# Kernel tuning notes

Hardware: AMD Instinct MI355X
Metric: run time of the kernel (lower is better)

Reference implementation:

```python
import jax, jax.numpy as jnp
import numpy as np


def setup_inputs() -> dict:
    key = jax.random.key(0)
    k1, k2 = jax.random.split(key)
    b, c, h, w = 16, 2048, 32, 32
    n_points = 64
    fea = jax.random.normal(k1, (b, c, h, w), dtype=jnp.float32)
    point_list = jax.random.uniform(k2, (n_points, 2), dtype=jnp.float32)  # (x, y) in [0,1)
    valid = jnp.ones((n_points,), dtype=bool)
    return {"fea": fea, "point_list": point_list, "valid": valid}


def reference(fea, point_list, valid):
    # forward_point of SimModel, with fea == backbone(x)['feat4']
    b, c, h, w = fea.shape
    # point_cur = [int(px*w), int(py*h)]  (points in [0,1) so trunc == floor)
    ix = jnp.clip((point_list[:, 0] * w).astype(jnp.int32), 0, w - 1)  # [P]
    iy = jnp.clip((point_list[:, 1] * h).astype(jnp.int32), 0, h - 1)  # [P]
    # gather query feature vectors at each point: [b, c, P]
    queries = fea[:, :, iy, ix]
    # cosine-normalize keys (over channel) and queries
    keys = fea / jnp.linalg.norm(fea, axis=1, keepdims=True)          # [b, c, h, w]
    q = queries / jnp.linalg.norm(queries, axis=1, keepdims=True)    # [b, c, P]
    # cosine-similarity attention over all h*w locations: [b, P, h*w]
    attn = jnp.einsum('bcp,bck->bpk', q, keys.reshape(b, c, h * w))
    # torch: attn = (attn - attn.min(-1)[0]) / attn.max(-1)[0]
    # (RHS fully evaluated first -> both min and max taken on the ORIGINAL attn)
    amin = attn.min(axis=-1, keepdims=True)
    amax = attn.max(axis=-1, keepdims=True)
    attn = (attn - amin) / amax
    soft_masks = attn.reshape(b, -1, h, w)                            # [b, P, h, w]
    # invalid points produce all-zero masks
    return jnp.where(valid[None, :, None, None], soft_masks, jnp.zeros((), soft_masks.dtype))
```

## Files before the change

kernel.cpp:

```cpp
#include <hip/hip_runtime.h>

#define BB 16
#define CC 2048
#define HH 32
#define WW 32
#define HW 1024
#define NP 64

#define PCH 32
#define NCH (CC/PCH)

#define KB 32
#define CT 32
#define NSTEP (CC/CT)

typedef __bf16 bf16x8 __attribute__((ext_vector_type(8)));
typedef float  f32x4  __attribute__((ext_vector_type(4)));

__device__ __forceinline__ unsigned f2bf2(float lo, float hi) {
    unsigned a = __float_as_uint(lo);
    unsigned b = __float_as_uint(hi);
    a += 0x7fffu + ((a >> 16) & 1u);
    b += 0x7fffu + ((b >> 16) & 1u);
    return (a >> 16) | (b & 0xffff0000u);
}


__global__ __launch_bounds__(256) void prep_kernel(const float* __restrict__ fea,
                                                   const float* __restrict__ pl,
                                                   unsigned short* __restrict__ qbf,
                                                   float* __restrict__ np2) {
    int cch = blockIdx.x, b = blockIdx.y;
    int t = threadIdx.x, lane = t & 63, rr = t >> 6;

    int ix = (int)(pl[2 * lane + 0] * WW); ix = min(max(ix, 0), WW - 1);
    int iy = (int)(pl[2 * lane + 1] * HH); iy = min(max(iy, 0), HH - 1);
    int kp = iy * WW + ix;

    __shared__ unsigned short buf[2][4][HW];
    __shared__ unsigned short ex[NP][PCH + 4];

    float ssq[16];
#pragma unroll
    for (int i = 0; i < 16; ++i) ssq[i] = 0.f;

    const float* base = fea + ((size_t)b * CC + cch * PCH + rr) * HW + 4 * lane;

#pragma unroll
    for (int ph = 0; ph < PCH / 4; ++ph) {
        float4 fv[4];
#pragma unroll
        for (int s = 0; s < 4; ++s)
            fv[s] = *(const float4*)(base + (size_t)(ph * 4) * HW + 256 * s);
#pragma unroll
        for (int s = 0; s < 4; ++s) {
            ssq[4 * s + 0] += fv[s].x * fv[s].x;
            ssq[4 * s + 1] += fv[s].y * fv[s].y;
            ssq[4 * s + 2] += fv[s].z * fv[s].z;
            ssq[4 * s + 3] += fv[s].w * fv[s].w;
            uint2 pk;
            pk.x = f2bf2(fv[s].x, fv[s].y);
            pk.y = f2bf2(fv[s].z, fv[s].w);
            *(uint2*)&buf[ph & 1][rr][4 * lane + 256 * s] = pk;
        }
        __syncthreads();
        ex[lane][ph * 4 + rr] = buf[ph & 1][rr][kp];
    }
    __syncthreads();

    float* red = (float*)buf;
#pragma unroll
    for (int s = 0; s < 4; ++s) {
        f32x4 v = {ssq[4 * s + 0], ssq[4 * s + 1], ssq[4 * s + 2], ssq[4 * s + 3]};
        *(f32x4*)&red[rr * HW + 4 * lane + 256 * s] = v;
    }
    __syncthreads();
    {
        int k0 = 4 * t;
        f32x4 r0 = *(f32x4*)&red[0 * HW + k0];
        f32x4 r1 = *(f32x4*)&red[1 * HW + k0];
        f32x4 r2 = *(f32x4*)&red[2 * HW + k0];
        f32x4 r3 = *(f32x4*)&red[3 * HW + k0];
        f32x4 sum = (r0 + r1) + (r2 + r3);
        *(f32x4*)&np2[((size_t)cch * BB + b) * HW + k0] = sum;
    }
    {
        int p = t >> 2, part = t & 3;
        uint2 lo = *(uint2*)&ex[p][8 * part];
        uint2 hi = *(uint2*)&ex[p][8 * part + 4];
        uint4 o = make_uint4(lo.x, lo.y, hi.x, hi.y);
        *(uint4*)&qbf[((size_t)b * NP + p) * CC + cch * PCH + 8 * part] = o;
    }
}

__global__ __launch_bounds__(128) void nred_kernel(const float* __restrict__ np2,
                                                   float* __restrict__ rn) {
    int b = blockIdx.y;
    int k = blockIdx.x * 128 + threadIdx.x;
    float s = 0.f;
#pragma unroll 8
    for (int cch = 0; cch < NCH; ++cch)
        s += np2[((size_t)cch * BB + b) * HW + k];
    rn[(size_t)b * HW + k] = rsqrtf(s);
}

__global__ __launch_bounds__(256) void gemm_kernel(const float* __restrict__ fea,
                                                   const unsigned short* __restrict__ qbf,
                                                   float* __restrict__ dot) {
    int id = blockIdx.x + (int)gridDim.x * blockIdx.y;
    int sid = (id & 7) * 64 + (id >> 3);
    int kc = sid & 31, b = sid >> 5;

    int t = threadIdx.x, lane = t & 63, w = t >> 6;
    int p0 = 16 * w, k0 = KB * kc;
    int gi = lane >> 4, ii = lane & 15;

    __shared__ __align__(16) unsigned short btT[2][KB][CT];

    int sk = t & 31, scg = t >> 5;
    int swz16 = (scg >> 1) ^ ((sk >> 1) & 3);
    unsigned short* wdst = &btT[0][sk][swz16 * 8 + (scg & 1) * 4];
    const float* gsrc = fea + ((size_t)b * CC + scg * 4) * HW + k0 + sk;

    const unsigned short* arow = qbf + ((size_t)b * NP + p0 + ii) * CC + 8 * gi;

    const unsigned short* brd = &btT[0][ii][(gi ^ ((ii >> 1) & 3)) * 8];

    f32x4 acc0 = {0.f, 0.f, 0.f, 0.f}, acc1 = {0.f, 0.f, 0.f, 0.f};
    union U8 { int4 i; bf16x8 v; };

    float g0 = gsrc[0 * HW], g1 = gsrc[1 * HW], g2 = gsrc[2 * HW], g3 = gsrc[3 * HW];
    U8 a_cur, a_nxt;
    a_cur.i = *(const int4*)arow;

    for (int s = 0; s < NSTEP; ++s) {
        int cur = s & 1;
        uint2 pk;
        pk.x = f2bf2(g0, g1);
        pk.y = f2bf2(g2, g3);
        *(uint2*)(wdst + cur * (KB * CT)) = pk;
        __syncthreads();

        int sn = (s + 1 < NSTEP) ? s + 1 : s;
        const float* gs = gsrc + (size_t)sn * CT * HW;
        g0 = gs[0 * HW]; g1 = gs[1 * HW]; g2 = gs[2 * HW]; g3 = gs[3 * HW];
        a_nxt.i = *(const int4*)(arow + sn * CT);

        const unsigned short* bp = brd + cur * (KB * CT);
        U8 b0, b1;
        b0.i = *(const int4*)bp;
        b1.i = *(const int4*)(bp + 16 * CT);
        acc0 = __builtin_amdgcn_mfma_f32_16x16x32_bf16(a_cur.v, b0.v, acc0, 0, 0, 0);
        acc1 = __builtin_amdgcn_mfma_f32_16x16x32_bf16(a_cur.v, b1.v, acc1, 0, 0, 0);
        a_cur = a_nxt;
    }

    float* dbase = dot + ((size_t)b * NP) * HW;
#pragma unroll
    for (int r = 0; r < 4; ++r) {
        int p = p0 + 4 * gi + r;
        dbase[(size_t)p * HW + k0 + ii]      = acc0[r];
        dbase[(size_t)p * HW + k0 + 16 + ii] = acc1[r];
    }
}

__global__ __launch_bounds__(256) void finalize_kernel(const float* __restrict__ dot,
                                                       const float* __restrict__ rn,
                                                       const float* __restrict__ pl,
                                                       const int* __restrict__ valid,
                                                       float* __restrict__ out) {
    int p = blockIdx.x, b = blockIdx.y;
    int t = threadIdx.x;
    int k0 = 4 * t;

    int ix = (int)(pl[2 * p + 0] * WW); ix = min(max(ix, 0), WW - 1);
    int iy = (int)(pl[2 * p + 1] * HH); iy = min(max(iy, 0), HH - 1);
    int kp = iy * WW + ix;
    float rnp = rn[(size_t)b * HW + kp];

    float4 d  = *(const float4*)&dot[((size_t)b * NP + p) * HW + k0];
    float4 rk = *(const float4*)&rn[(size_t)b * HW + k0];

    float val[4];
    val[0] = d.x * rk.x * rnp;
    val[1] = d.y * rk.y * rnp;
    val[2] = d.z * rk.z * rnp;
    val[3] = d.w * rk.w * rnp;

    float mn = fminf(fminf(val[0], val[1]), fminf(val[2], val[3]));
    float mx = fmaxf(fmaxf(val[0], val[1]), fmaxf(val[2], val[3]));
#pragma unroll
    for (int off = 32; off; off >>= 1) {
        mn = fminf(mn, __shfl_xor(mn, off));
        mx = fmaxf(mx, __shfl_xor(mx, off));
    }
    __shared__ float smn[4], smx[4];
    int wave = t >> 6;
    if ((t & 63) == 0) { smn[wave] = mn; smx[wave] = mx; }
    __syncthreads();
    mn = fminf(fminf(smn[0], smn[1]), fminf(smn[2], smn[3]));
    mx = fmaxf(fmaxf(smx[0], smx[1]), fmaxf(smx[2], smx[3]));

    bool vld = valid[p] != 0;
    float4 o;
    o.x = vld ? (val[0] - mn) / mx : 0.f;
    o.y = vld ? (val[1] - mn) / mx : 0.f;
    o.z = vld ? (val[2] - mn) / mx : 0.f;
    o.w = vld ? (val[3] - mn) / mx : 0.f;
    *(float4*)&out[((size_t)b * NP + p) * HW + k0] = o;
}

extern "C" void kernel_launch(void* const* d_in, const int* in_sizes, int n_in,
                              void* d_out, int out_size, void* d_ws, size_t ws_size,
                              hipStream_t stream) {
    const float* fea = (const float*)d_in[0];
    const float* pl  = (const float*)d_in[1];
    const int* valid = (const int*)d_in[2];
    float* out = (float*)d_out;

    unsigned short* qbf = (unsigned short*)d_ws;
    float* np2 = (float*)(qbf + (size_t)BB * NP * CC);
    float* rn  = np2 + (size_t)NCH * BB * HW;
    float* dot = rn + (size_t)BB * HW;

    prep_kernel<<<dim3(NCH, BB), 256, 0, stream>>>(fea, pl, qbf, np2);
    nred_kernel<<<dim3(8, BB), 128, 0, stream>>>(np2, rn);
    gemm_kernel<<<dim3(HW / KB, BB), 256, 0, stream>>>(fea, qbf, dot);
    finalize_kernel<<<dim3(NP, BB), 256, 0, stream>>>(dot, rn, pl, valid, out);
}
```

Baseline: 65.71 us.

## Restructure GEMM to split-K over channel halves with wider tiles and B reuse

The GEMM now gives each block a 64-wide spatial tile and half of the channel range (split-K by 2), and the two partial dot products are summed in the finalize kernel. Each wave holds a 16-column slice of B and loops over all 64 points, reading A directly from global memory, so each B fragment is reused four times. Stores into shared memory use an XOR swizzle, and global fea loads become float4. In exchange it writes twice the partial-dot traffic, reads B from LDS with scalar 16-bit gathers, and adds a second barrier per step.

```diff
diff --git a/kernel.cpp b/kernel.cpp
--- a/kernel.cpp
+++ b/kernel.cpp
@@ -10,9 +10,11 @@
 #define PCH 32
 #define NCH (CC/PCH)
 
-#define KB 32
-#define CT 32
-#define NSTEP (CC/CT)
+#define KB 64
+#define CT 64
+#define CS 2
+#define CHALF (CC/CS)
+#define NSTEP (CHALF/CT)
 
 typedef __bf16 bf16x8 __attribute__((ext_vector_type(8)));
 typedef float  f32x4  __attribute__((ext_vector_type(4)));
@@ -106,65 +108,86 @@
 
 __global__ __launch_bounds__(256) void gemm_kernel(const float* __restrict__ fea,
                                                    const unsigned short* __restrict__ qbf,
-                                                   float* __restrict__ dot) {
+                                                   float* __restrict__ dotp) {
     int id = blockIdx.x + (int)gridDim.x * blockIdx.y;
     int sid = (id & 7) * 64 + (id >> 3);
-    int kc = sid & 31, b = sid >> 5;
+    int kc = sid & 15, cs = (sid >> 4) & 1, b = sid >> 5;
 
     int t = threadIdx.x, lane = t & 63, w = t >> 6;
-    int p0 = 16 * w, k0 = KB * kc;
     int gi = lane >> 4, ii = lane & 15;
-
-    __shared__ __align__(16) unsigned short btT[2][KB][CT];
-
-    int sk = t & 31, scg = t >> 5;
-    int swz16 = (scg >> 1) ^ ((sk >> 1) & 3);
-    unsigned short* wdst = &btT[0][sk][swz16 * 8 + (scg & 1) * 4];
-    const float* gsrc = fea + ((size_t)b * CC + scg * 4) * HW + k0 + sk;
-
-    const unsigned short* arow = qbf + ((size_t)b * NP + p0 + ii) * CC + 8 * gi;
-
-    const unsigned short* brd = &btT[0][ii][(gi ^ ((ii >> 1) & 3)) * 8];
-
-    f32x4 acc0 = {0.f, 0.f, 0.f, 0.f}, acc1 = {0.f, 0.f, 0.f, 0.f};
-    union U8 { int4 i; bf16x8 v; };
-
-    float g0 = gsrc[0 * HW], g1 = gsrc[1 * HW], g2 = gsrc[2 * HW], g3 = gsrc[3 * HW];
-    U8 a_cur, a_nxt;
-    a_cur.i = *(const int4*)arow;
+    int k0 = KB * kc;
+    int c0 = cs * CHALF;
+
+    __shared__ __align__(16) unsigned short bt[2][CT][KB];
+
+    int sc = t >> 2, sq = t & 3;
+    const float* gsrc = fea + ((size_t)b * CC + c0 + sc) * HW + k0 + 4 * sq;
+
+    const unsigned short* qb = qbf + (size_t)b * NP * CC + c0;
+
+    f32x4 acc[4];
+#pragma unroll
+    for (int pt = 0; pt < 4; ++pt) acc[pt] = (f32x4){0.f, 0.f, 0.f, 0.f};
+
+    union UA { int4 i; bf16x8 v; };
+
+    float4 g[4];
+#pragma unroll
+    for (int h = 0; h < 4; ++h) g[h] = *(const float4*)(gsrc + 16 * h);
+
+    int kb2 = 4 * w + (ii >> 2);
+    int klo = ii & 3;
 
     for (int s = 0; s < NSTEP; ++s) {
         int cur = s & 1;
-        uint2 pk;
-        pk.x = f2bf2(g0, g1);
-        pk.y = f2bf2(g2, g3);
-        *(uint2*)(wdst + cur * (KB * CT)) = pk;
+#pragma unroll
+        for (int h = 0; h < 4; ++h) {
+            int sw = ((4 * h + sq) ^ (sc & 15)) & 15;
+            uint2 pk;
+            pk.x = f2bf2(g[h].x, g[h].y);
+            pk.y = f2bf2(g[h].z, g[h].w);
+            *(uint2*)&bt[cur][sc][sw * 4] = pk;
+        }
         __syncthreads();
 
         int sn = (s + 1 < NSTEP) ? s + 1 : s;
-        const float* gs = gsrc + (size_t)sn * CT * HW;
-        g0 = gs[0 * HW]; g1 = gs[1 * HW]; g2 = gs[2 * HW]; g3 = gs[3 * HW];
-        a_nxt.i = *(const int4*)(arow + sn * CT);
-
-        const unsigned short* bp = brd + cur * (KB * CT);
-        U8 b0, b1;
-        b0.i = *(const int4*)bp;
-        b1.i = *(const int4*)(bp + 16 * CT);
-        acc0 = __builtin_amdgcn_mfma_f32_16x16x32_bf16(a_cur.v, b0.v, acc0, 0, 0, 0);
-        acc1 = __builtin_amdgcn_mfma_f32_16x16x32_bf16(a_cur.v, b1.v, acc1, 0, 0, 0);
-        a_cur = a_nxt;
-    }
-
-    float* dbase = dot + ((size_t)b * NP) * HW;
-#pragma unroll
-    for (int r = 0; r < 4; ++r) {
-        int p = p0 + 4 * gi + r;
-        dbase[(size_t)p * HW + k0 + ii]      = acc0[r];
-        dbase[(size_t)p * HW + k0 + 16 + ii] = acc1[r];
-    }
-}
-
-__global__ __launch_bounds__(256) void finalize_kernel(const float* __restrict__ dot,
+#pragma unroll
+        for (int h = 0; h < 4; ++h)
+            g[h] = *(const float4*)(gsrc + (size_t)sn * CT * HW + 16 * h);
+
+#pragma unroll
+        for (int cw = 0; cw < 2; ++cw) {
+            union { unsigned short u[8]; bf16x8 v; } bf;
+            int swb = kb2 ^ (8 * (gi & 1));
+#pragma unroll
+            for (int e = 0; e < 8; ++e) {
+                int c = cw * 32 + 8 * gi + e;
+                int sw = (swb ^ e) & 15;
+                bf.u[e] = bt[cur][c][sw * 4 + klo];
+            }
+#pragma unroll
+            for (int pt = 0; pt < 4; ++pt) {
+                UA a;
+                a.i = *(const int4*)(qb + (size_t)(16 * pt + ii) * CC
+                                     + s * CT + cw * 32 + 8 * gi);
+                acc[pt] = __builtin_amdgcn_mfma_f32_16x16x32_bf16(a.v, bf.v, acc[pt], 0, 0, 0);
+            }
+        }
+        __syncthreads();
+    }
+
+    float* dbase = dotp + (((size_t)cs * BB + b) * NP) * HW;
+#pragma unroll
+    for (int pt = 0; pt < 4; ++pt) {
+#pragma unroll
+        for (int r = 0; r < 4; ++r) {
+            int p = 16 * pt + 4 * gi + r;
+            dbase[(size_t)p * HW + k0 + 16 * w + ii] = acc[pt][r];
+        }
+    }
+}
+
+__global__ __launch_bounds__(256) void finalize_kernel(const float* __restrict__ dotp,
                                                        const float* __restrict__ rn,
                                                        const float* __restrict__ pl,
                                                        const int* __restrict__ valid,
@@ -178,14 +201,17 @@
     int kp = iy * WW + ix;
     float rnp = rn[(size_t)b * HW + kp];
 
-    float4 d  = *(const float4*)&dot[((size_t)b * NP + p) * HW + k0];
+    const float* d0p = dotp + (((size_t)0 * BB + b) * NP + p) * HW;
+    const float* d1p = dotp + (((size_t)1 * BB + b) * NP + p) * HW;
+    float4 d0 = *(const float4*)(d0p + k0);
+    float4 d1 = *(const float4*)(d1p + k0);
     float4 rk = *(const float4*)&rn[(size_t)b * HW + k0];
 
     float val[4];
-    val[0] = d.x * rk.x * rnp;
-    val[1] = d.y * rk.y * rnp;
-    val[2] = d.z * rk.z * rnp;
-    val[3] = d.w * rk.w * rnp;
+    val[0] = (d0.x + d1.x) * rk.x * rnp;
+    val[1] = (d0.y + d1.y) * rk.y * rnp;
+    val[2] = (d0.z + d1.z) * rk.z * rnp;
+    val[3] = (d0.w + d1.w) * rk.w * rnp;
 
     float mn = fminf(fminf(val[0], val[1]), fminf(val[2], val[3]));
     float mx = fmaxf(fmaxf(val[0], val[1]), fmaxf(val[2], val[3]));
@@ -221,10 +247,10 @@
     unsigned short* qbf = (unsigned short*)d_ws;
     float* np2 = (float*)(qbf + (size_t)BB * NP * CC);
     float* rn  = np2 + (size_t)NCH * BB * HW;
-    float* dot = rn + (size_t)BB * HW;
+    float* dotp = rn + (size_t)BB * HW;
 
     prep_kernel<<<dim3(NCH, BB), 256, 0, stream>>>(fea, pl, qbf, np2);
     nred_kernel<<<dim3(8, BB), 128, 0, stream>>>(np2, rn);
-    gemm_kernel<<<dim3(HW / KB, BB), 256, 0, stream>>>(fea, qbf, dot);
-    finalize_kernel<<<dim3(NP, BB), 256, 0, stream>>>(dot, rn, pl, valid, out);
-}
+    gemm_kernel<<<dim3(16 * CS, BB), 256, 0, stream>>>(fea, qbf, dotp);
+    finalize_kernel<<<dim3(NP, BB), 256, 0, stream>>>(dotp, rn, pl, valid, out);
+}
```

Result: slower. 73.29 us (+11.5%).
